# Performance work log

Hardware: AMD Instinct MI355X
Metric: run time of the kernel (lower is better)

## Reference

```python
import jax, jax.numpy as jnp
import numpy as np
import math

K_S = 2  # graph power order
K_T = 2  # temporal localization copies
BN_EPS = 1e-5


def setup_inputs() -> dict:
    key = jax.random.key(0)
    ks = jax.random.split(key, 12)
    B, L, N, H, ND = 8, 12, 1024, 32, 16
    AF = H + ND  # all_feat_dim
    return {
        "history_data": jax.random.normal(ks[0], (B, L, N, 1), jnp.float32),
        "node_embedding_d": jax.random.normal(ks[1], (N, ND), jnp.float32),
        "node_embedding_u": jax.random.normal(ks[2], (N, ND), jnp.float32),
        "adj0": jax.random.uniform(ks[3], (N, N), jnp.float32),
        "adj1": jax.random.uniform(ks[4], (N, N), jnp.float32),
        "W1": jax.random.normal(ks[5], (L, 2 * H), jnp.float32) * 0.1,
        "b1": jnp.zeros((2 * H,), jnp.float32),
        "gamma": jnp.ones((2 * H,), jnp.float32),
        "beta": jnp.zeros((2 * H,), jnp.float32),
        "W2": jax.random.normal(ks[6], (2 * H, H), jnp.float32) * 0.1,
        "b2": jnp.zeros((H,), jnp.float32),
        "WQ": jax.random.normal(ks[7], (AF, H), jnp.float32) * 0.1,
        "WK": jax.random.normal(ks[8], (AF, H), jnp.float32) * 0.1,
    }


def _forward(history_data, node_embedding_d, node_embedding_u, adj0, adj1,
             W1, b1, gamma, beta, W2, b2, WQ, WK):
    B, L, N, _ = history_data.shape
    H = W2.shape[1]

    # --- DistanceFunction ---
    X = jnp.transpose(history_data[..., 0], (0, 2, 1)).reshape(B * N, L)  # [B*N, L]
    h = jax.nn.relu(X @ W1 + b1)                                          # [B*N, 2H]
    mu = jnp.mean(h, axis=0)
    var = jnp.var(h, axis=0)  # biased, matches torch BatchNorm1d train norm
    h = (h - mu) * jax.lax.rsqrt(var + BN_EPS) * gamma + beta
    dy_feat = (h @ W2 + b2).reshape(B, N, H)                              # [B, N, H]

    scale = 1.0 / math.sqrt(H)
    adjs = []
    for emb in (node_embedding_d, node_embedding_u):
        feat = jnp.concatenate(
            [dy_feat, jnp.broadcast_to(emb[None], (B,) + emb.shape)], axis=-1)
        Q = feat @ WQ  # [B, N, H]
        K = feat @ WK
        logits = jnp.einsum("bnh,bmh->bnm", Q, K) * scale
        adjs.append(jax.nn.softmax(logits, axis=-1))

    # --- Mask ---
    adjs = [(adj0 + 1e-7)[None] * adjs[0], (adj1 + 1e-7)[None] * adjs[1]]

    # --- Normalizer: diag_embed+bmm is just a row-wise broadcast scale ---
    def norm(g):
        inv = 1.0 / jnp.sum(g, axis=2)
        inv = jnp.where(jnp.isfinite(inv), inv, 0.0)
        return inv[:, :, None] * g
    adjs = [norm(g) for g in adjs]

    # --- MultiOrder (k=1..K_S), zero diagonal ---
    offdiag = 1.0 - jnp.eye(N, dtype=adjs[0].dtype)
    graphs = []
    for g in adjs:
        k_order = g
        graphs.append(k_order * offdiag)
        for _ in range(2, K_S + 1):
            k_order = jnp.einsum("bnm,bmk->bnk", k_order, g)
            graphs.append(k_order * offdiag)

    # --- st_localization: [B,N,N] -> [B,N,K_T*N] (row repeated K_T times) ---
    local = [jnp.broadcast_to(g[:, :, None, :], (B, N, K_T, N)).reshape(B, N, K_T * N)
             for g in graphs]
    return jnp.stack(local, axis=0)  # [2*K_S, B, N, K_T*N]


def reference(history_data, node_embedding_d, node_embedding_u, adj0, adj1,
              W1, b1, gamma, beta, W2, b2, WQ, WK):
    return _forward(history_data, node_embedding_d, node_embedding_u, adj0, adj1,
                    W1, b1, gamma, beta, W2, b2, WQ, WK)
```

## Files before the change

### kernel.cpp

```cpp
#include <hip/hip_runtime.h>

typedef unsigned short u16;
typedef unsigned int   u32;

typedef __bf16 bf16x8 __attribute__((ext_vector_type(8)));
typedef float  f32x4  __attribute__((ext_vector_type(4)));

__device__ __forceinline__ float bf2f(u16 u) {
  u32 x = ((u32)u) << 16; float f; __builtin_memcpy(&f, &x, 4); return f;
}
__device__ __forceinline__ u16 f2bf(float f) {
  u32 x; __builtin_memcpy(&x, &f, 4);
  x += 0x7fffu + ((x >> 16) & 1u);
  return (u16)(x >> 16);
}
__device__ __forceinline__ void gl2lds16(const void* g, void* l) {
  __builtin_amdgcn_global_load_lds((const __attribute__((address_space(1))) void*)g,
                                   (__attribute__((address_space(3))) void*)l, 16, 0, 0);
}

__global__ __launch_bounds__(256) void k_h(const float* __restrict__ hd, const float* __restrict__ W1,
                                           const float* __restrict__ b1, float* __restrict__ h)
{
  __shared__ float w1s[12 * 64];
  __shared__ float b1s[64];
  int t = threadIdx.x;
  for (int idx = t; idx < 768; idx += 256) w1s[idx] = W1[idx];
  if (t < 64) b1s[t] = b1[t];
  __syncthreads();
  int i = blockIdx.x * 256 + t;
  int b = i >> 10, n = i & 1023;
  float x[12];
#pragma unroll
  for (int l = 0; l < 12; ++l) x[l] = hd[(b * 12 + l) * 1024 + n];
  float acc[64];
#pragma unroll
  for (int j = 0; j < 64; ++j) acc[j] = b1s[j];
#pragma unroll
  for (int l = 0; l < 12; ++l) {
    float xl = x[l];
#pragma unroll
    for (int j = 0; j < 64; ++j) acc[j] += xl * w1s[l * 64 + j];
  }
  float4* hv = (float4*)(h + (size_t)i * 64);
#pragma unroll
  for (int j4 = 0; j4 < 16; ++j4) {
    float4 v;
    v.x = fmaxf(acc[j4 * 4 + 0], 0.f);
    v.y = fmaxf(acc[j4 * 4 + 1], 0.f);
    v.z = fmaxf(acc[j4 * 4 + 2], 0.f);
    v.w = fmaxf(acc[j4 * 4 + 3], 0.f);
    hv[j4] = v;
  }
}

__global__ __launch_bounds__(256) void k_stats(const float* __restrict__ h, float* __restrict__ stats)
{
  int t = threadIdx.x;
  size_t base = (size_t)blockIdx.x * 8192;
  float s = 0.f, sq = 0.f;
  for (int it = 0; it < 32; ++it) {
    float v = h[base + it * 256 + t];
    s += v; sq += v * v;
  }
  __shared__ float ls[256], lq[256];
  ls[t] = s; lq[t] = sq;
  __syncthreads();
  if (t < 64) {
    float S = ls[t] + ls[t + 64] + ls[t + 128] + ls[t + 192];
    float Q = lq[t] + lq[t + 64] + lq[t + 128] + lq[t + 192];
    atomicAdd(&stats[t], S);
    atomicAdd(&stats[64 + t], Q);
  }
}

__global__ void k_finalize(const float* __restrict__ stats, const float* __restrict__ gamma,
                           const float* __restrict__ beta, float* __restrict__ ss)
{
  int t = threadIdx.x;
  float mu = stats[t] * (1.f / 8192.f);
  float var = stats[64 + t] * (1.f / 8192.f) - mu * mu;
  float inv = rsqrtf(var + 1e-5f);
  float sc = gamma[t] * inv;
  ss[t] = sc;
  ss[64 + t] = beta[t] - mu * sc;
}

__global__ __launch_bounds__(256) void k_emb(const float* __restrict__ embd, const float* __restrict__ embu,
                                             const float* __restrict__ WQ, const float* __restrict__ WK,
                                             float* __restrict__ embpart)
{
  int g = blockIdx.x * 256 + threadIdx.x;
  int o = g & 31, n = (g >> 5) & 1023, qk = (g >> 15) & 1, e = g >> 16;
  const float* emb = e ? embu : embd;
  const float* W = qk ? WK : WQ;
  float acc = 0.f;
#pragma unroll
  for (int d = 0; d < 16; ++d) acc += emb[n * 16 + d] * W[(32 + d) * 32 + o];
  embpart[g] = acc;
}

__global__ __launch_bounds__(256) void k_dyqk(const float* __restrict__ h, const float* __restrict__ ss,
                                              const float* __restrict__ W2, const float* __restrict__ b2,
                                              const float* __restrict__ WQ, const float* __restrict__ WK,
                                              const float* __restrict__ embpart,
                                              float* __restrict__ QTf, u16* __restrict__ KTb)
{
  __shared__ float w2s[64 * 32], wqs[32 * 32], wks[32 * 32], b2s[32], scs[64], shs[64];
  int t = threadIdx.x;
  for (int idx = t; idx < 2048; idx += 256) w2s[idx] = W2[idx];
  for (int idx = t; idx < 1024; idx += 256) { wqs[idx] = WQ[idx]; wks[idx] = WK[idx]; }
  if (t < 32) b2s[t] = b2[t];
  if (t < 64) { scs[t] = ss[t]; shs[t] = ss[64 + t]; }
  __syncthreads();
  int i = blockIdx.x * 256 + t;
  int b = i >> 10, n = i & 1023;
  float dy[32];
#pragma unroll
  for (int o = 0; o < 32; ++o) dy[o] = b2s[o];
  for (int j = 0; j < 64; ++j) {
    float hj = h[(size_t)i * 64 + j] * scs[j] + shs[j];
#pragma unroll
    for (int o = 0; o < 32; ++o) dy[o] += hj * w2s[j * 32 + o];
  }
  float tq[32], tk[32];
#pragma unroll
  for (int o = 0; o < 32; ++o) { tq[o] = 0.f; tk[o] = 0.f; }
  for (int j = 0; j < 32; ++j) {
    float d = dy[j];
#pragma unroll
    for (int o = 0; o < 32; ++o) { tq[o] += d * wqs[j * 32 + o]; tk[o] += d * wks[j * 32 + o]; }
  }
#pragma unroll
  for (int e = 0; e < 2; ++e) {
    const float* epQ = embpart + ((size_t)(e * 2 + 0) * 1024 + n) * 32;
    const float* epK = embpart + ((size_t)(e * 2 + 1) * 1024 + n) * 32;
    size_t qb = ((size_t)(e * 8 + b) * 32) * 1024 + n;
#pragma unroll
    for (int o = 0; o < 32; ++o) {
      QTf[qb + (size_t)o * 1024] = tq[o] + epQ[o];
      KTb[qb + (size_t)o * 1024] = f2bf(tk[o] + epK[o]);
    }
  }
}

__global__ __launch_bounds__(256) void k_attn(const float* __restrict__ QTf, const u16* __restrict__ KTb,
                                              const float* __restrict__ adj0, const float* __restrict__ adj1,
                                              u16* __restrict__ G, float* __restrict__ out)
{
  int blk = (blockIdx.x & 7) * 64 + (blockIdx.x >> 3);
  int rg = blk & 31, b = (blk >> 5) & 7, e = blk >> 8;
  int t = threadIdx.x;
  int eb = e * 8 + b;
  int wv = t >> 6, lane = t & 63;
  const float* adj = e ? adj1 : adj0;
  const u16* Kp = KTb + ((size_t)eb << 15);
  const float* Qp = QTf + ((size_t)eb << 15);
  u16* Gp = G + ((size_t)eb << 20);
  float* o1 = out + (((size_t)(2 * e) * 8 + b) << 21);
  const float sc = 0.17677669529663687f;
#pragma unroll
  for (int grp = 0; grp < 2; ++grp) {
    int r0 = rg * 32 + wv * 8 + grp * 4;
    float accA[4][8], accB[4][8];
#pragma unroll
    for (int r = 0; r < 4; ++r)
#pragma unroll
      for (int k = 0; k < 8; ++k) { accA[r][k] = 0.f; accB[r][k] = 0.f; }
    for (int hh = 0; hh < 32; ++hh) {
      float4 qv = *(const float4*)(Qp + hh * 1024 + r0);
      uint4 ka = *(const uint4*)(Kp + hh * 1024 + lane * 8);
      uint4 kb = *(const uint4*)(Kp + hh * 1024 + 512 + lane * 8);
      float kf[8] = {bf2f((u16)ka.x), bf2f((u16)(ka.x >> 16)), bf2f((u16)ka.y), bf2f((u16)(ka.y >> 16)),
                     bf2f((u16)ka.z), bf2f((u16)(ka.z >> 16)), bf2f((u16)ka.w), bf2f((u16)(ka.w >> 16))};
      float kg[8] = {bf2f((u16)kb.x), bf2f((u16)(kb.x >> 16)), bf2f((u16)kb.y), bf2f((u16)(kb.y >> 16)),
                     bf2f((u16)kb.z), bf2f((u16)(kb.z >> 16)), bf2f((u16)kb.w), bf2f((u16)(kb.w >> 16))};
#pragma unroll
      for (int k = 0; k < 8; ++k) {
        accA[0][k] += qv.x * kf[k]; accA[1][k] += qv.y * kf[k];
        accA[2][k] += qv.z * kf[k]; accA[3][k] += qv.w * kf[k];
        accB[0][k] += qv.x * kg[k]; accB[1][k] += qv.y * kg[k];
        accB[2][k] += qv.z * kg[k]; accB[3][k] += qv.w * kg[k];
      }
    }
#pragma unroll
    for (int r = 0; r < 4; ++r) {
      int gr = r0 + r;
      const float* arow = adj + ((size_t)gr << 10);
      int mA = lane * 8, mB = 512 + lane * 8;
      float4 a0 = *(const float4*)(arow + mA);
      float4 a1 = *(const float4*)(arow + mA + 4);
      float4 c0 = *(const float4*)(arow + mB);
      float4 c1 = *(const float4*)(arow + mB + 4);
      float af[8] = {a0.x, a0.y, a0.z, a0.w, a1.x, a1.y, a1.z, a1.w};
      float bfv[8] = {c0.x, c0.y, c0.z, c0.w, c1.x, c1.y, c1.z, c1.w};
      float ta[8], tb[8];
      float p = 0.f;
#pragma unroll
      for (int k = 0; k < 8; ++k) { ta[k] = (af[k] + 1e-7f) * __expf(accA[r][k] * sc); p += ta[k]; }
#pragma unroll
      for (int k = 0; k < 8; ++k) { tb[k] = (bfv[k] + 1e-7f) * __expf(accB[r][k] * sc); p += tb[k]; }
#pragma unroll
      for (int off = 32; off > 0; off >>= 1) p += __shfl_xor(p, off);
      float inv = 1.f / p;
      if (!__builtin_isfinite(inv)) inv = 0.f;
      float ga[8], gb[8];
#pragma unroll
      for (int k = 0; k < 8; ++k) { ga[k] = ta[k] * inv; gb[k] = tb[k] * inv; }
      uint4 pa, pb;
      pa.x = f2bf(ga[0]) | ((u32)f2bf(ga[1]) << 16);  pa.y = f2bf(ga[2]) | ((u32)f2bf(ga[3]) << 16);
      pa.z = f2bf(ga[4]) | ((u32)f2bf(ga[5]) << 16);  pa.w = f2bf(ga[6]) | ((u32)f2bf(ga[7]) << 16);
      pb.x = f2bf(gb[0]) | ((u32)f2bf(gb[1]) << 16);  pb.y = f2bf(gb[2]) | ((u32)f2bf(gb[3]) << 16);
      pb.z = f2bf(gb[4]) | ((u32)f2bf(gb[5]) << 16);  pb.w = f2bf(gb[6]) | ((u32)f2bf(gb[7]) << 16);
      *(uint4*)(Gp + ((size_t)gr << 10) + mA) = pa;
      *(uint4*)(Gp + ((size_t)gr << 10) + mB) = pb;
#pragma unroll
      for (int k = 0; k < 8; ++k) {
        if (mA + k == gr) ga[k] = 0.f;
        if (mB + k == gr) gb[k] = 0.f;
      }
      size_t ob = (size_t)gr << 11;
      float4 fa0 = {ga[0], ga[1], ga[2], ga[3]}, fa1 = {ga[4], ga[5], ga[6], ga[7]};
      float4 fb0 = {gb[0], gb[1], gb[2], gb[3]}, fb1 = {gb[4], gb[5], gb[6], gb[7]};
      *(float4*)(o1 + ob + mA) = fa0;         *(float4*)(o1 + ob + mA + 4) = fa1;
      *(float4*)(o1 + ob + mB) = fb0;         *(float4*)(o1 + ob + mB + 4) = fb1;
      *(float4*)(o1 + ob + 1024 + mA) = fa0;  *(float4*)(o1 + ob + 1024 + mA + 4) = fa1;
      *(float4*)(o1 + ob + 1024 + mB) = fb0;  *(float4*)(o1 + ob + 1024 + mB + 4) = fb1;
    }
  }
}

__global__ __launch_bounds__(256) void k_tr(const u16* __restrict__ G, u16* __restrict__ Gt)
{
  __shared__ u16 tile[64 * 66];
  int blk = blockIdx.x;
  int mat = blk >> 8, tl = blk & 255, ti = tl >> 4, tj = tl & 15;
  size_t mo = (size_t)mat << 20;
  int t = threadIdx.x;
#pragma unroll
  for (int half = 0; half < 2; ++half) {
    int idx = t + half * 256;
    int row = idx >> 3, q = idx & 7;
    uint4 v = *(const uint4*)(G + mo + (size_t)(ti * 64 + row) * 1024 + tj * 64 + q * 8);
    u16* d = &tile[row * 66 + q * 8];
    d[0] = (u16)v.x; d[1] = (u16)(v.x >> 16);
    d[2] = (u16)v.y; d[3] = (u16)(v.y >> 16);
    d[4] = (u16)v.z; d[5] = (u16)(v.z >> 16);
    d[6] = (u16)v.w; d[7] = (u16)(v.w >> 16);
  }
  __syncthreads();
#pragma unroll
  for (int half = 0; half < 2; ++half) {
    int idx = t + half * 256;
    int row = idx >> 3, q = idx & 7;
    u16 s0 = tile[(q * 8 + 0) * 66 + row], s1 = tile[(q * 8 + 1) * 66 + row];
    u16 s2 = tile[(q * 8 + 2) * 66 + row], s3 = tile[(q * 8 + 3) * 66 + row];
    u16 s4 = tile[(q * 8 + 4) * 66 + row], s5 = tile[(q * 8 + 5) * 66 + row];
    u16 s6 = tile[(q * 8 + 6) * 66 + row], s7 = tile[(q * 8 + 7) * 66 + row];
    uint4 v;
    v.x = s0 | ((u32)s1 << 16); v.y = s2 | ((u32)s3 << 16);
    v.z = s4 | ((u32)s5 << 16); v.w = s6 | ((u32)s7 << 16);
    *(uint4*)(Gt + mo + (size_t)(tj * 64 + row) * 1024 + ti * 64 + q * 8) = v;
  }
}

__global__ __launch_bounds__(256) void k_gemm(const u16* __restrict__ G, const u16* __restrict__ Gt,
                                              float* __restrict__ out)
{
  __shared__ __align__(16) u16 As[2][128 * 32];
  __shared__ __align__(16) u16 Bs[2][128 * 32];
  int bid = (blockIdx.x & 7) * 128 + (blockIdx.x >> 3);
  int mat = bid >> 6, tile = bid & 63, ti = tile >> 3, tj = tile & 7;
  size_t mo = (size_t)mat << 20;
  const u16* A = G + mo;
  const u16* Bm = Gt + mo;
  int t = threadIdx.x;
  int w = t >> 6, lane = t & 63;
  int quad = lane >> 4, l16 = lane & 15;
  int wr = (w & 1) * 64, wc = (w >> 1) * 64;
  int srow = lane >> 2, scol = lane & 3;
  f32x4 acc[4][4];
#pragma unroll
  for (int i = 0; i < 4; ++i)
#pragma unroll
    for (int j = 0; j < 4; ++j) acc[i][j] = f32x4{0.f, 0.f, 0.f, 0.f};

#define STAGE(buf, kk)                                                                  \
  {                                                                                     \
    _Pragma("unroll")                                                                   \
    for (int it = 0; it < 2; ++it) {                                                    \
      int sbase = (it * 4 + w) * 64;                                                    \
      int r = (sbase + lane) >> 2, c = (sbase + lane) & 3;                              \
      gl2lds16(A + (size_t)(ti * 128 + r) * 1024 + (kk) + c * 8,                        \
               (u16*)As[buf] + (size_t)sbase * 8);                                      \
      gl2lds16(Bm + (size_t)(tj * 128 + r) * 1024 + (kk) + c * 8,                       \
               (u16*)Bs[buf] + (size_t)sbase * 8);                                      \
    }                                                                                   \
  }

  STAGE(0, 0);
  __syncthreads();
  int cur = 0;
  for (int k0 = 0; k0 < 1024; k0 += 32) {
    if (k0 + 32 < 1024) STAGE(cur ^ 1, k0 + 32);
    bf16x8 af[4], bfr[4];
#pragma unroll
    for (int mt = 0; mt < 4; ++mt)
      af[mt] = *(const bf16x8*)&As[cur][(wr + mt * 16 + l16) * 32 + quad * 8];
#pragma unroll
    for (int nt = 0; nt < 4; ++nt)
      bfr[nt] = *(const bf16x8*)&Bs[cur][(wc + nt * 16 + l16) * 32 + quad * 8];
#pragma unroll
    for (int mt = 0; mt < 4; ++mt)
#pragma unroll
      for (int nt = 0; nt < 4; ++nt)
        acc[mt][nt] = __builtin_amdgcn_mfma_f32_16x16x32_bf16(af[mt], bfr[nt], acc[mt][nt], 0, 0, 0);
    __syncthreads();
    cur ^= 1;
  }
#undef STAGE
  (void)srow; (void)scol;
  int e = mat >> 3, bb = mat & 7;
  float* o2 = out + (((size_t)(2 * e + 1) * 8 + bb) << 21);
#pragma unroll
  for (int mt = 0; mt < 4; ++mt)
#pragma unroll
    for (int r = 0; r < 4; ++r) {
      int gr = ti * 128 + wr + mt * 16 + quad * 4 + r;
      size_t rb = (size_t)gr << 11;
#pragma unroll
      for (int nt = 0; nt < 4; ++nt) {
        int gc = tj * 128 + wc + nt * 16 + l16;
        float v = (gr == gc) ? 0.f : acc[mt][nt][r];
        o2[rb + gc] = v;
        o2[rb + 1024 + gc] = v;
      }
    }
}

extern "C" void kernel_launch(void* const* d_in, const int* in_sizes, int n_in,
                              void* d_out, int out_size, void* d_ws, size_t ws_size,
                              hipStream_t stream) {
  const float* hd    = (const float*)d_in[0];
  const float* embd  = (const float*)d_in[1];
  const float* embu  = (const float*)d_in[2];
  const float* adj0  = (const float*)d_in[3];
  const float* adj1  = (const float*)d_in[4];
  const float* W1    = (const float*)d_in[5];
  const float* b1    = (const float*)d_in[6];
  const float* gamma = (const float*)d_in[7];
  const float* beta  = (const float*)d_in[8];
  const float* W2    = (const float*)d_in[9];
  const float* b2    = (const float*)d_in[10];
  const float* WQ    = (const float*)d_in[11];
  const float* WK    = (const float*)d_in[12];
  char* ws = (char*)d_ws;
  float* stats   = (float*)(ws + 0);
  float* ss      = (float*)(ws + 1024);
  float* embpart = (float*)(ws + 4096);
  float* h       = (float*)(ws + 528384);
  float* QTf     = (float*)(ws + 2625536);
  u16* KTb       = (u16*)(ws + 4722688);
  u16* G         = (u16*)(ws + 5771264);
  u16* Gt        = (u16*)(ws + 39325696);
  float* out     = (float*)d_out;

  hipMemsetAsync(stats, 0, 512, stream);
  k_h<<<32, 256, 0, stream>>>(hd, W1, b1, h);
  k_stats<<<64, 256, 0, stream>>>(h, stats);
  k_finalize<<<1, 64, 0, stream>>>(stats, gamma, beta, ss);
  k_emb<<<512, 256, 0, stream>>>(embd, embu, WQ, WK, embpart);
  k_dyqk<<<32, 256, 0, stream>>>(h, ss, W2, b2, WQ, WK, embpart, QTf, KTb);
  k_attn<<<512, 256, 0, stream>>>(QTf, KTb, adj0, adj1, G, out);
  k_tr<<<4096, 256, 0, stream>>>(G, Gt);
  k_gemm<<<1024, 256, 0, stream>>>(G, Gt, out);
}
```

Measured before the change: 416.0 us.

## Transpose h layout, merge BN stats/finalize, fold embedding projection into dyqk

Writes the ReLU output in feature-major layout so a single per-feature kernel can compute batch-norm statistics and scale/shift without atomics or a memset. The separate finalize and embedding-projection kernels are removed, and the embedding part of the Q/K projection is computed inside k_dyqk. This cuts the prologue from six launches to three, at the cost of strided per-feature stores in k_h and extra per-thread FMAs in k_dyqk. The prologue is small next to the attention and GEMM kernels.

Result: slower. 609.3 us (+46.5%).

```diff
diff --git a/kernel.cpp b/kernel.cpp
--- a/kernel.cpp
+++ b/kernel.cpp
@@ -20,7 +20,7 @@
 }
 
 __global__ __launch_bounds__(256) void k_h(const float* __restrict__ hd, const float* __restrict__ W1,
-                                           const float* __restrict__ b1, float* __restrict__ h)
+                                           const float* __restrict__ b1, float* __restrict__ hT)
 {
   __shared__ float w1s[12 * 64];
   __shared__ float b1s[64];
@@ -42,74 +42,51 @@
 #pragma unroll
     for (int j = 0; j < 64; ++j) acc[j] += xl * w1s[l * 64 + j];
   }
-  float4* hv = (float4*)(h + (size_t)i * 64);
-#pragma unroll
-  for (int j4 = 0; j4 < 16; ++j4) {
-    float4 v;
-    v.x = fmaxf(acc[j4 * 4 + 0], 0.f);
-    v.y = fmaxf(acc[j4 * 4 + 1], 0.f);
-    v.z = fmaxf(acc[j4 * 4 + 2], 0.f);
-    v.w = fmaxf(acc[j4 * 4 + 3], 0.f);
-    hv[j4] = v;
-  }
-}
-
-__global__ __launch_bounds__(256) void k_stats(const float* __restrict__ h, float* __restrict__ stats)
-{
-  int t = threadIdx.x;
-  size_t base = (size_t)blockIdx.x * 8192;
-  float s = 0.f, sq = 0.f;
+#pragma unroll
+  for (int j = 0; j < 64; ++j) hT[(size_t)j * 8192 + i] = fmaxf(acc[j], 0.f);
+}
+
+__global__ __launch_bounds__(256) void k_bn(const float* __restrict__ hT, const float* __restrict__ gamma,
+                                            const float* __restrict__ beta, float* __restrict__ ss)
+{
+  int j = blockIdx.x;
+  int t = threadIdx.x;
+  const float* row = hT + (size_t)j * 8192;
+  float s = 0.f, q = 0.f;
   for (int it = 0; it < 32; ++it) {
-    float v = h[base + it * 256 + t];
-    s += v; sq += v * v;
+    float v = row[it * 256 + t];
+    s += v; q += v * v;
   }
   __shared__ float ls[256], lq[256];
-  ls[t] = s; lq[t] = sq;
-  __syncthreads();
-  if (t < 64) {
-    float S = ls[t] + ls[t + 64] + ls[t + 128] + ls[t + 192];
-    float Q = lq[t] + lq[t + 64] + lq[t + 128] + lq[t + 192];
-    atomicAdd(&stats[t], S);
-    atomicAdd(&stats[64 + t], Q);
-  }
-}
-
-__global__ void k_finalize(const float* __restrict__ stats, const float* __restrict__ gamma,
-                           const float* __restrict__ beta, float* __restrict__ ss)
-{
-  int t = threadIdx.x;
-  float mu = stats[t] * (1.f / 8192.f);
-  float var = stats[64 + t] * (1.f / 8192.f) - mu * mu;
-  float inv = rsqrtf(var + 1e-5f);
-  float sc = gamma[t] * inv;
-  ss[t] = sc;
-  ss[64 + t] = beta[t] - mu * sc;
-}
-
-__global__ __launch_bounds__(256) void k_emb(const float* __restrict__ embd, const float* __restrict__ embu,
-                                             const float* __restrict__ WQ, const float* __restrict__ WK,
-                                             float* __restrict__ embpart)
-{
-  int g = blockIdx.x * 256 + threadIdx.x;
-  int o = g & 31, n = (g >> 5) & 1023, qk = (g >> 15) & 1, e = g >> 16;
-  const float* emb = e ? embu : embd;
-  const float* W = qk ? WK : WQ;
-  float acc = 0.f;
-#pragma unroll
-  for (int d = 0; d < 16; ++d) acc += emb[n * 16 + d] * W[(32 + d) * 32 + o];
-  embpart[g] = acc;
-}
-
-__global__ __launch_bounds__(256) void k_dyqk(const float* __restrict__ h, const float* __restrict__ ss,
+  ls[t] = s; lq[t] = q;
+  __syncthreads();
+  for (int off = 128; off > 0; off >>= 1) {
+    if (t < off) { ls[t] += ls[t + off]; lq[t] += lq[t + off]; }
+    __syncthreads();
+  }
+  if (t == 0) {
+    float mu = ls[0] * (1.f / 8192.f);
+    float var = lq[0] * (1.f / 8192.f) - mu * mu;
+    float inv = rsqrtf(var + 1e-5f);
+    float sc = gamma[j] * inv;
+    ss[j] = sc;
+    ss[64 + j] = beta[j] - mu * sc;
+  }
+}
+
+__global__ __launch_bounds__(256) void k_dyqk(const float* __restrict__ hT, const float* __restrict__ ss,
                                               const float* __restrict__ W2, const float* __restrict__ b2,
                                               const float* __restrict__ WQ, const float* __restrict__ WK,
-                                              const float* __restrict__ embpart,
+                                              const float* __restrict__ embd, const float* __restrict__ embu,
                                               float* __restrict__ QTf, u16* __restrict__ KTb)
 {
-  __shared__ float w2s[64 * 32], wqs[32 * 32], wks[32 * 32], b2s[32], scs[64], shs[64];
+  __shared__ float w2s[64 * 32], wqs[32 * 32], wks[32 * 32];
+  __shared__ float wqe[16 * 32], wke[16 * 32];
+  __shared__ float b2s[32], scs[64], shs[64];
   int t = threadIdx.x;
   for (int idx = t; idx < 2048; idx += 256) w2s[idx] = W2[idx];
   for (int idx = t; idx < 1024; idx += 256) { wqs[idx] = WQ[idx]; wks[idx] = WK[idx]; }
+  for (int idx = t; idx < 512; idx += 256) { wqe[idx] = WQ[1024 + idx]; wke[idx] = WK[1024 + idx]; }
   if (t < 32) b2s[t] = b2[t];
   if (t < 64) { scs[t] = ss[t]; shs[t] = ss[64 + t]; }
   __syncthreads();
@@ -119,7 +96,7 @@
 #pragma unroll
   for (int o = 0; o < 32; ++o) dy[o] = b2s[o];
   for (int j = 0; j < 64; ++j) {
-    float hj = h[(size_t)i * 64 + j] * scs[j] + shs[j];
+    float hj = hT[(size_t)j * 8192 + i] * scs[j] + shs[j];
 #pragma unroll
     for (int o = 0; o < 32; ++o) dy[o] += hj * w2s[j * 32 + o];
   }
@@ -133,13 +110,18 @@
   }
 #pragma unroll
   for (int e = 0; e < 2; ++e) {
-    const float* epQ = embpart + ((size_t)(e * 2 + 0) * 1024 + n) * 32;
-    const float* epK = embpart + ((size_t)(e * 2 + 1) * 1024 + n) * 32;
+    const float* emb = e ? embu : embd;
+    float em[16];
+#pragma unroll
+    for (int d = 0; d < 16; ++d) em[d] = emb[n * 16 + d];
     size_t qb = ((size_t)(e * 8 + b) * 32) * 1024 + n;
 #pragma unroll
     for (int o = 0; o < 32; ++o) {
-      QTf[qb + (size_t)o * 1024] = tq[o] + epQ[o];
-      KTb[qb + (size_t)o * 1024] = f2bf(tk[o] + epK[o]);
+      float eq = 0.f, ek = 0.f;
+#pragma unroll
+      for (int d = 0; d < 16; ++d) { eq += em[d] * wqe[d * 32 + o]; ek += em[d] * wke[d * 32 + o]; }
+      QTf[qb + (size_t)o * 1024] = tq[o] + eq;
+      KTb[qb + (size_t)o * 1024] = f2bf(tk[o] + ek);
     }
   }
 }
@@ -278,7 +260,6 @@
   int w = t >> 6, lane = t & 63;
   int quad = lane >> 4, l16 = lane & 15;
   int wr = (w & 1) * 64, wc = (w >> 1) * 64;
-  int srow = lane >> 2, scol = lane & 3;
   f32x4 acc[4][4];
 #pragma unroll
   for (int i = 0; i < 4; ++i)
@@ -319,7 +300,6 @@
     cur ^= 1;
   }
 #undef STAGE
-  (void)srow; (void)scol;
   int e = mat >> 3, bb = mat & 7;
   float* o2 = out + (((size_t)(2 * e + 1) * 8 + bb) << 21);
 #pragma unroll
@@ -355,22 +335,17 @@
   const float* WQ    = (const float*)d_in[11];
   const float* WK    = (const float*)d_in[12];
   char* ws = (char*)d_ws;
-  float* stats   = (float*)(ws + 0);
   float* ss      = (float*)(ws + 1024);
-  float* embpart = (float*)(ws + 4096);
-  float* h       = (float*)(ws + 528384);
+  float* hT      = (float*)(ws + 528384);
   float* QTf     = (float*)(ws + 2625536);
   u16* KTb       = (u16*)(ws + 4722688);
   u16* G         = (u16*)(ws + 5771264);
   u16* Gt        = (u16*)(ws + 39325696);
   float* out     = (float*)d_out;
 
-  hipMemsetAsync(stats, 0, 512, stream);
-  k_h<<<32, 256, 0, stream>>>(hd, W1, b1, h);
-  k_stats<<<64, 256, 0, stream>>>(h, stats);
-  k_finalize<<<1, 64, 0, stream>>>(stats, gamma, beta, ss);
-  k_emb<<<512, 256, 0, stream>>>(embd, embu, WQ, WK, embpart);
-  k_dyqk<<<32, 256, 0, stream>>>(h, ss, W2, b2, WQ, WK, embpart, QTf, KTb);
+  k_h<<<32, 256, 0, stream>>>(hd, W1, b1, hT);
+  k_bn<<<64, 256, 0, stream>>>(hT, gamma, beta, ss);
+  k_dyqk<<<32, 256, 0, stream>>>(hT, ss, W2, b2, WQ, WK, embd, embu, QTf, KTb);
   k_attn<<<512, 256, 0, stream>>>(QTf, KTb, adj0, adj1, G, out);
   k_tr<<<4096, 256, 0, stream>>>(G, Gt);
   k_gemm<<<1024, 256, 0, stream>>>(G, Gt, out);
```
